# Kernel optimization log

Hardware: AMD Instinct MI355X
Metric: run time of the kernel (lower is better)

Reference implementation:

```python
import jax, jax.numpy as jnp
import numpy as np

E_SIZE, IN_SIZE = 16, 8
PROJ = 8 + IN_SIZE  # 16
H = 1  # hidden_size hardcoded in the module


def setup_inputs() -> dict:
    key = jax.random.key(0)
    ks = jax.random.split(key, 6)
    W, E, B, I, F = 64, E_SIZE, 256, 10, IN_SIZE
    inputs = jax.random.normal(ks[0], (W, E, B, I, F), dtype=jnp.float32)
    state = jnp.zeros((1, E, B * I, H), dtype=jnp.float32)
    # parameters (xavier/orthogonal init approximated with scaled normals)
    wl_scale = float(np.sqrt(2.0 / (PROJ + F)))
    wih_scale = float(np.sqrt(2.0 / (3 * H + PROJ)))
    weight_linear = jax.random.normal(ks[1], (E, PROJ, F), dtype=jnp.float32) * wl_scale
    bias_linear = jnp.zeros((E, PROJ), dtype=jnp.float32)
    weight_ih = jax.random.normal(ks[2], (E, 3 * H, PROJ), dtype=jnp.float32) * wih_scale
    weight_hh = jax.random.normal(ks[3], (E, 3 * H, H), dtype=jnp.float32)  # orthogonal-ish (H=1 -> +-1 scale ok)
    bias_ih = jnp.zeros((E, 3 * H), dtype=jnp.float32)
    bias_hh = jnp.zeros((E, 3 * H), dtype=jnp.float32)
    return {"inputs": inputs, "state": state, "weight_linear": weight_linear,
            "bias_linear": bias_linear, "weight_ih": weight_ih, "weight_hh": weight_hh,
            "bias_ih": bias_ih, "bias_hh": bias_hh}


def reference(inputs, state, weight_linear, bias_linear, weight_ih, weight_hh, bias_ih, bias_hh):
    W, E, B, I, F = inputs.shape
    x = inputs.reshape(W, E, B * I, F)
    h0 = state[-1].reshape(E, B * I, H)
    # linear projection: (E,proj,F) x (W,E,BI,F) -> (W,E,BI,proj)
    y = jnp.einsum('eoi,webi->webo', weight_linear, x) + bias_linear[:, None, :]
    # input-to-hidden gates precomputed for all timesteps: (W,E,BI,3)
    gi_all = jnp.einsum('ego,webo->webg', weight_ih, y) + bias_ih[:, None, :]

    def step(h, gi):
        gh = jnp.einsum('ego,ebo->ebg', weight_hh, h) + bias_hh[:, None, :]
        r = jax.nn.sigmoid(gi[..., :H] + gh[..., :H])
        z = jax.nn.sigmoid(gi[..., H:2 * H] + gh[..., H:2 * H])
        n = jnp.tanh(gi[..., 2 * H:] + r * gh[..., 2 * H:])
        h = (1 - z) * n + z * h
        return h, h

    _, outs = jax.lax.scan(step, h0, gi_all)  # (W,E,BI,1)
    return outs.reshape(W, E, B, I, 1)
```

## Files before the change

kernel.cpp:

```cpp
#include <hip/hip_runtime.h>


namespace {
constexpr int W_T = 64;
constexpr int E_N = 16;
constexpr int B_N = 256;
constexpr int I_N = 10;
constexpr int F_N = 8;
constexpr int PROJ = 16;
constexpr int BI = B_N * I_N;
constexpr int WSTRIDE = E_N * BI * F_N;
constexpr int OSTRIDE = E_N * BI;
constexpr int NCHAIN = E_N * BI;
constexpr int BLOCKS_PER_E = BI / 64;

__device__ __forceinline__ float sigmoid_f(float x) {
    return __frcp_rn(1.f + __expf(-x));
}
__device__ __forceinline__ float tanh_f(float x) {
    return __builtin_fmaf(-2.f, __frcp_rn(1.f + __expf(2.f * x)), 1.f);
}
}

__global__ __launch_bounds__(64, 1) void EnsembleGRUModule_63213328662935_kernel(
    const float* __restrict__ x,
    const float* __restrict__ h0p,
    const float* __restrict__ wl,
    const float* __restrict__ bl,
    const float* __restrict__ wih,
    const float* __restrict__ whh,
    const float* __restrict__ bih,
    const float* __restrict__ bhh,
    float* __restrict__ out)
{
    const int e = blockIdx.x / BLOCKS_PER_E;
    const int bi = (blockIdx.x % BLOCKS_PER_E) * 64 + threadIdx.x;
    const int chain = e * BI + bi;

    const float* wl_e = wl + e * (PROJ * F_N);
    const float* wih_e = wih + e * (3 * PROJ);
    float M[3][F_N];
    float c[3];
    #pragma unroll
    for (int g = 0; g < 3; ++g) {
        float cg = bih[e * 3 + g];
        float m[F_N];
        #pragma unroll
        for (int f = 0; f < F_N; ++f) m[f] = 0.f;
        #pragma unroll
        for (int o = 0; o < PROJ; ++o) {
            const float wgo = wih_e[g * PROJ + o];
            cg = __builtin_fmaf(wgo, bl[e * PROJ + o], cg);
            #pragma unroll
            for (int f = 0; f < F_N; ++f)
                m[f] = __builtin_fmaf(wgo, wl_e[o * F_N + f], m[f]);
        }
        #pragma unroll
        for (int f = 0; f < F_N; ++f) M[g][f] = m[f];
        c[g] = cg;
    }
    const float w0 = whh[e * 3 + 0], w1 = whh[e * 3 + 1], w2 = whh[e * 3 + 2];
    const float c0 = c[0] + bhh[e * 3 + 0];
    const float c1 = c[1] + bhh[e * 3 + 1];
    const float c2 = c[2];
    const float bh2 = bhh[e * 3 + 2];

    const float* xp = x + (size_t)chain * F_N;
    float* op = out + chain;
    float h = h0p[chain];

    constexpr int CH = 8;
    constexpr int NC = W_T / CH;
    float4 buf[2][CH][2];

    #pragma unroll
    for (int j = 0; j < CH; ++j) {
        buf[0][j][0] = *(const float4*)(xp + (size_t)j * WSTRIDE);
        buf[0][j][1] = *(const float4*)(xp + (size_t)j * WSTRIDE + 4);
    }

    #pragma unroll
    for (int chunk = 0; chunk < NC; ++chunk) {
        const int cur = chunk & 1;
        if (chunk + 1 < NC) {
            #pragma unroll
            for (int j = 0; j < CH; ++j) {
                const size_t off = (size_t)((chunk + 1) * CH + j) * WSTRIDE;
                buf[cur ^ 1][j][0] = *(const float4*)(xp + off);
                buf[cur ^ 1][j][1] = *(const float4*)(xp + off + 4);
            }
        }
        #pragma unroll
        for (int j = 0; j < CH; ++j) {
            const float4 A = buf[cur][j][0];
            const float4 Bv = buf[cur][j][1];
            const float xv[8] = {A.x, A.y, A.z, A.w, Bv.x, Bv.y, Bv.z, Bv.w};
            float g0 = c0, g1 = c1, g2 = c2;
            #pragma unroll
            for (int f = 0; f < 8; ++f) {
                g0 = __builtin_fmaf(M[0][f], xv[f], g0);
                g1 = __builtin_fmaf(M[1][f], xv[f], g1);
                g2 = __builtin_fmaf(M[2][f], xv[f], g2);
            }
            const float r = sigmoid_f(__builtin_fmaf(w0, h, g0));
            const float z = sigmoid_f(__builtin_fmaf(w1, h, g1));
            const float gh2 = __builtin_fmaf(w2, h, bh2);
            const float n = tanh_f(__builtin_fmaf(r, gh2, g2));
            h = __builtin_fmaf(z, h - n, n);
            op[(size_t)(chunk * CH + j) * OSTRIDE] = h;
        }
    }
}

extern "C" void kernel_launch(void* const* d_in, const int* in_sizes, int n_in,
                              void* d_out, int out_size, void* d_ws, size_t ws_size,
                              hipStream_t stream) {
    const float* x   = (const float*)d_in[0];
    const float* st  = (const float*)d_in[1];
    const float* wl  = (const float*)d_in[2];
    const float* bl  = (const float*)d_in[3];
    const float* wih = (const float*)d_in[4];
    const float* whh = (const float*)d_in[5];
    const float* bih = (const float*)d_in[6];
    const float* bhh = (const float*)d_in[7];
    float* out = (float*)d_out;

    dim3 grid(NCHAIN / 64);
    dim3 block(64);
    hipLaunchKernelGGL(EnsembleGRUModule_63213328662935_kernel, grid, block, 0, stream,
                       x, st, wl, bl, wih, whh, bih, bhh, out);
}
```

Baseline: 135.8 us.

## Split GRU into fold, fully parallel gate-precompute, and sequential scan kernels

Replaces the single fused kernel with three kernels. A tiny kernel folds the linear and input-hidden weights together with the exp2 scaling. A massively parallel kernel computes the input gates for all timesteps into workspace. A 64-thread-per-block scan kernel then reads the precomputed gates and runs the recurrence with exp2/rcp intrinsics. The aim is to take the input projection off the latency-bound serial chain and let it run at full occupancy, at the cost of extra global traffic to write and reread the gate buffer (three floats per step versus eight inputs) and two extra launches.

```diff
diff --git a/kernel.cpp b/kernel.cpp
--- a/kernel.cpp
+++ b/kernel.cpp
@@ -4,112 +4,134 @@
 namespace {
 constexpr int W_T = 64;
 constexpr int E_N = 16;
-constexpr int B_N = 256;
-constexpr int I_N = 10;
 constexpr int F_N = 8;
 constexpr int PROJ = 16;
-constexpr int BI = B_N * I_N;
-constexpr int WSTRIDE = E_N * BI * F_N;
-constexpr int OSTRIDE = E_N * BI;
-constexpr int NCHAIN = E_N * BI;
-constexpr int BLOCKS_PER_E = BI / 64;
-
-__device__ __forceinline__ float sigmoid_f(float x) {
-    return __frcp_rn(1.f + __expf(-x));
-}
-__device__ __forceinline__ float tanh_f(float x) {
-    return __builtin_fmaf(-2.f, __frcp_rn(1.f + __expf(2.f * x)), 1.f);
-}
+constexpr int BI = 2560;
+constexpr int OST = E_N * BI;
+constexpr int TOT = W_T * OST;
+constexpr int BLOCKS_PER_W = OST / 256;
+constexpr int BLOCKS_PER_E_SCAN = BI / 64;
+constexpr float L2E = 1.44269504088896340736f;
+constexpr int MC_STRIDE = 12;
+constexpr size_t MC_BYTES = 4096;
 }
 
-__global__ __launch_bounds__(64, 1) void EnsembleGRUModule_63213328662935_kernel(
+__global__ void gru_fold_kernel(const float* __restrict__ wl,
+                                const float* __restrict__ bl,
+                                const float* __restrict__ wih,
+                                const float* __restrict__ whh,
+                                const float* __restrict__ bih,
+                                const float* __restrict__ bhh,
+                                float* __restrict__ mc)
+{
+    const int t = threadIdx.x;
+    if (t >= E_N * 3) return;
+    const int e = t / 3, g = t % 3;
+    const float* wl_e = wl + e * (PROJ * F_N);
+    const float* wih_eg = wih + e * (3 * PROJ) + g * PROJ;
+    float m[F_N];
+    #pragma unroll
+    for (int f = 0; f < F_N; ++f) m[f] = 0.f;
+    float c = bih[e * 3 + g];
+    #pragma unroll
+    for (int o = 0; o < PROJ; ++o) {
+        const float wgo = wih_eg[o];
+        c = __builtin_fmaf(wgo, bl[e * PROJ + o], c);
+        #pragma unroll
+        for (int f = 0; f < F_N; ++f)
+            m[f] = __builtin_fmaf(wgo, wl_e[o * F_N + f], m[f]);
+    }
+    const float scale = (g == 2) ? (2.f * L2E) : (-L2E);
+    float* p = mc + (e * 3 + g) * MC_STRIDE;
+    #pragma unroll
+    for (int f = 0; f < F_N; ++f) p[f] = scale * m[f];
+    p[8] = (g == 2) ? scale * c : scale * (c + bhh[e * 3 + g]);
+    p[9] = scale * whh[e * 3 + g];
+    p[10] = (g == 2) ? scale * bhh[e * 3 + 2] : 0.f;
+    p[11] = 0.f;
+}
+
+__global__ __launch_bounds__(256) void gru_gi_kernel(
     const float* __restrict__ x,
+    const float* __restrict__ mc,
+    float* __restrict__ gi)
+{
+    const int b = blockIdx.x;
+    const int w = b / BLOCKS_PER_W;
+    const int e = (b % BLOCKS_PER_W) / 10;
+    const int idx = b * 256 + (int)threadIdx.x;
+    const int chain = idx - w * OST;
+
+    const float* mcp = mc + e * (3 * MC_STRIDE);
+    const float4 A4 = *(const float4*)(x + (size_t)idx * F_N);
+    const float4 B4 = *(const float4*)(x + (size_t)idx * F_N + 4);
+    const float xv[8] = {A4.x, A4.y, A4.z, A4.w, B4.x, B4.y, B4.z, B4.w};
+
+    float a0 = mcp[8], a1 = mcp[MC_STRIDE + 8], a2 = mcp[2 * MC_STRIDE + 8];
+    #pragma unroll
+    for (int f = 0; f < F_N; ++f) {
+        a0 = __builtin_fmaf(mcp[f], xv[f], a0);
+        a1 = __builtin_fmaf(mcp[MC_STRIDE + f], xv[f], a1);
+        a2 = __builtin_fmaf(mcp[2 * MC_STRIDE + f], xv[f], a2);
+    }
+    gi[(size_t)(w * 3 + 0) * OST + chain] = a0;
+    gi[(size_t)(w * 3 + 1) * OST + chain] = a1;
+    gi[(size_t)(w * 3 + 2) * OST + chain] = a2;
+}
+
+__global__ __launch_bounds__(64, 1) void gru_scan_kernel(
+    const float* __restrict__ gi,
     const float* __restrict__ h0p,
-    const float* __restrict__ wl,
-    const float* __restrict__ bl,
-    const float* __restrict__ wih,
-    const float* __restrict__ whh,
-    const float* __restrict__ bih,
-    const float* __restrict__ bhh,
+    const float* __restrict__ mc,
     float* __restrict__ out)
 {
-    const int e = blockIdx.x / BLOCKS_PER_E;
-    const int bi = (blockIdx.x % BLOCKS_PER_E) * 64 + threadIdx.x;
-    const int chain = e * BI + bi;
+    const int e = blockIdx.x / BLOCKS_PER_E_SCAN;
+    const int chain = blockIdx.x * 64 + (int)threadIdx.x;
 
-    const float* wl_e = wl + e * (PROJ * F_N);
-    const float* wih_e = wih + e * (3 * PROJ);
-    float M[3][F_N];
-    float c[3];
-    #pragma unroll
-    for (int g = 0; g < 3; ++g) {
-        float cg = bih[e * 3 + g];
-        float m[F_N];
-        #pragma unroll
-        for (int f = 0; f < F_N; ++f) m[f] = 0.f;
-        #pragma unroll
-        for (int o = 0; o < PROJ; ++o) {
-            const float wgo = wih_e[g * PROJ + o];
-            cg = __builtin_fmaf(wgo, bl[e * PROJ + o], cg);
-            #pragma unroll
-            for (int f = 0; f < F_N; ++f)
-                m[f] = __builtin_fmaf(wgo, wl_e[o * F_N + f], m[f]);
-        }
-        #pragma unroll
-        for (int f = 0; f < F_N; ++f) M[g][f] = m[f];
-        c[g] = cg;
-    }
-    const float w0 = whh[e * 3 + 0], w1 = whh[e * 3 + 1], w2 = whh[e * 3 + 2];
-    const float c0 = c[0] + bhh[e * 3 + 0];
-    const float c1 = c[1] + bhh[e * 3 + 1];
-    const float c2 = c[2];
-    const float bh2 = bhh[e * 3 + 2];
+    const float* mcp = mc + e * (3 * MC_STRIDE);
+    const float W0s = mcp[9];
+    const float W1s = mcp[MC_STRIDE + 9];
+    const float W2s = mcp[2 * MC_STRIDE + 9];
+    const float bh2s = mcp[2 * MC_STRIDE + 10];
 
-    const float* xp = x + (size_t)chain * F_N;
-    float* op = out + chain;
     float h = h0p[chain];
 
-    constexpr int CH = 8;
-    constexpr int NC = W_T / CH;
-    float4 buf[2][CH][2];
+    constexpr int CH2 = 16;
+    float g0A[CH2], g1A[CH2], g2A[CH2], g0B[CH2], g1B[CH2], g2B[CH2];
 
-    #pragma unroll
-    for (int j = 0; j < CH; ++j) {
-        buf[0][j][0] = *(const float4*)(xp + (size_t)j * WSTRIDE);
-        buf[0][j][1] = *(const float4*)(xp + (size_t)j * WSTRIDE + 4);
-    }
+    auto LOAD = [&](float (&g0)[CH2], float (&g1)[CH2], float (&g2)[CH2], int c) {
+        #pragma unroll
+        for (int j = 0; j < CH2; ++j) {
+            const int t = c * CH2 + j;
+            g0[j] = gi[(size_t)(t * 3 + 0) * OST + chain];
+            g1[j] = gi[(size_t)(t * 3 + 1) * OST + chain];
+            g2[j] = gi[(size_t)(t * 3 + 2) * OST + chain];
+        }
+    };
+    auto COMP = [&](const float (&g0)[CH2], const float (&g1)[CH2],
+                    const float (&g2)[CH2], int c) {
+        #pragma unroll
+        for (int j = 0; j < CH2; ++j) {
+            const float r = __builtin_amdgcn_rcpf(
+                1.f + __builtin_amdgcn_exp2f(__builtin_fmaf(W0s, h, g0[j])));
+            const float z = __builtin_amdgcn_rcpf(
+                1.f + __builtin_amdgcn_exp2f(__builtin_fmaf(W1s, h, g1[j])));
+            const float t2 = __builtin_fmaf(r, __builtin_fmaf(W2s, h, bh2s), g2[j]);
+            const float n = __builtin_fmaf(
+                -2.f, __builtin_amdgcn_rcpf(1.f + __builtin_amdgcn_exp2f(t2)), 1.f);
+            h = __builtin_fmaf(z, h - n, n);
+            out[(size_t)(c * CH2 + j) * OST + chain] = h;
+        }
+    };
 
-    #pragma unroll
-    for (int chunk = 0; chunk < NC; ++chunk) {
-        const int cur = chunk & 1;
-        if (chunk + 1 < NC) {
-            #pragma unroll
-            for (int j = 0; j < CH; ++j) {
-                const size_t off = (size_t)((chunk + 1) * CH + j) * WSTRIDE;
-                buf[cur ^ 1][j][0] = *(const float4*)(xp + off);
-                buf[cur ^ 1][j][1] = *(const float4*)(xp + off + 4);
-            }
-        }
-        #pragma unroll
-        for (int j = 0; j < CH; ++j) {
-            const float4 A = buf[cur][j][0];
-            const float4 Bv = buf[cur][j][1];
-            const float xv[8] = {A.x, A.y, A.z, A.w, Bv.x, Bv.y, Bv.z, Bv.w};
-            float g0 = c0, g1 = c1, g2 = c2;
-            #pragma unroll
-            for (int f = 0; f < 8; ++f) {
-                g0 = __builtin_fmaf(M[0][f], xv[f], g0);
-                g1 = __builtin_fmaf(M[1][f], xv[f], g1);
-                g2 = __builtin_fmaf(M[2][f], xv[f], g2);
-            }
-            const float r = sigmoid_f(__builtin_fmaf(w0, h, g0));
-            const float z = sigmoid_f(__builtin_fmaf(w1, h, g1));
-            const float gh2 = __builtin_fmaf(w2, h, bh2);
-            const float n = tanh_f(__builtin_fmaf(r, gh2, g2));
-            h = __builtin_fmaf(z, h - n, n);
-            op[(size_t)(chunk * CH + j) * OSTRIDE] = h;
-        }
-    }
+    LOAD(g0A, g1A, g2A, 0);
+    LOAD(g0B, g1B, g2B, 1);
+    COMP(g0A, g1A, g2A, 0);
+    LOAD(g0A, g1A, g2A, 2);
+    COMP(g0B, g1B, g2B, 1);
+    LOAD(g0B, g1B, g2B, 3);
+    COMP(g0A, g1A, g2A, 2);
+    COMP(g0B, g1B, g2B, 3);
 }
 
 extern "C" void kernel_launch(void* const* d_in, const int* in_sizes, int n_in,
@@ -125,8 +147,13 @@
     const float* bhh = (const float*)d_in[7];
     float* out = (float*)d_out;
 
-    dim3 grid(NCHAIN / 64);
-    dim3 block(64);
-    hipLaunchKernelGGL(EnsembleGRUModule_63213328662935_kernel, grid, block, 0, stream,
-                       x, st, wl, bl, wih, whh, bih, bhh, out);
+    float* mc = (float*)d_ws;
+    float* gi = (float*)((char*)d_ws + MC_BYTES);
+
+    hipLaunchKernelGGL(gru_fold_kernel, dim3(1), dim3(64), 0, stream,
+                       wl, bl, wih, whh, bih, bhh, mc);
+    hipLaunchKernelGGL(gru_gi_kernel, dim3(TOT / 256), dim3(256), 0, stream,
+                       x, mc, gi);
+    hipLaunchKernelGGL(gru_scan_kernel, dim3(OST / 64), dim3(64), 0, stream,
+                       gi, st, mc, out);
 }
```

Result: slower. 148.8 us (+9.5%).
